# Performance work log

Hardware: AMD Instinct MI355X
Metric: run time of the kernel (lower is better)

The kernel has to match this reference:

```python
import jax, jax.numpy as jnp
import numpy as np

B, N, D = 16, 4096, 64  # (batch*heads, seq_len, head_dim)

def setup_inputs() -> dict:
    key = jax.random.key(0)
    kq, kk, kv = jax.random.split(key, 3)
    queries = jax.random.normal(kq, (B, N, D), dtype=jnp.float32)
    keys = jax.random.normal(kk, (B, N, D), dtype=jnp.float32)
    values = jax.random.normal(kv, (B, N, D), dtype=jnp.float32)
    masking = jnp.zeros((B, N), dtype=jnp.float32)
    return {"queries": queries, "keys": keys, "values": values, "masking": masking}

def reference(queries, keys, values, masking):
    # Faithful to source: masks() computes the additive mask but returns
    # `inputs` unchanged (bug in original), so `masking` is a no-op.
    d = queries.shape[-1]
    scores = jnp.einsum('bnd,bmd->bnm', queries, keys) / jnp.sqrt(jnp.float32(d))
    attn = jax.nn.softmax(scores, axis=-1)
    # Dropout(rate=0) at inference is identity.
    out = jnp.einsum('bnm,bmd->bnd', attn, values)
    return out
```

## Files before the change

### kernel.cpp

```cpp
#include <hip/hip_runtime.h>
#include <hip/hip_bf16.h>

#define B_    16
#define N_    4096
#define D_    64
#define QBLK  256
#define KVBLK 64
#define KTILES (N_ / KVBLK)

typedef __attribute__((ext_vector_type(8))) short short8v;
typedef __attribute__((ext_vector_type(4))) float f32x4;
typedef __attribute__((ext_vector_type(4))) unsigned uint4v;

__device__ __forceinline__ short f2bf(float x) {
    union { float f; unsigned u; } c; c.f = x;
    unsigned r = c.u + 0x7FFFu + ((c.u >> 16) & 1u);
    return (short)(r >> 16);
}
__device__ __forceinline__ unsigned cvtpk(float lo, float hi) {
    unsigned r;
    asm("v_cvt_pk_bf16_f32 %0, %1, %2" : "=v"(r) : "v"(lo), "v"(hi));
    return r;
}
__device__ __forceinline__ float fexp2(float x) {
    float r;
    asm("v_exp_f32 %0, %1" : "=v"(r) : "v"(x));
    return r;
}

#define GLDS16(g, l)                                                      \
    __builtin_amdgcn_global_load_lds(                                     \
        (const __attribute__((address_space(1))) void*)(g),               \
        (__attribute__((address_space(3))) void*)(l), 16, 0, 0)

__global__ __launch_bounds__(256) void conv_k(const float* __restrict__ K,
                                              short* __restrict__ Kp) {
    const int idx  = blockIdx.x * 256 + threadIdx.x;
    const int nout = idx >> 3;
    const int c8   = (idx & 7) << 3;
    const int p    = nout & 63;
    const int sig  = (p & 3) | (((p >> 4) & 1) << 2) |
                     (((p >> 2) & 3) << 3) | ((p >> 5) << 5);
    const int nsrc = (nout & ~63) | sig;
    const float* src = K + (size_t)nsrc * D_ + c8;
    const f32x4 a = *(const f32x4*)src;
    const f32x4 b = *(const f32x4*)(src + 4);
    short8v o;
    o[0] = f2bf(a[0]); o[1] = f2bf(a[1]); o[2] = f2bf(a[2]); o[3] = f2bf(a[3]);
    o[4] = f2bf(b[0]); o[5] = f2bf(b[1]); o[6] = f2bf(b[2]); o[7] = f2bf(b[3]);
    const int cs = c8 ^ ((p & 7) << 3);
    *(short8v*)(Kp + (size_t)nout * D_ + cs) = o;
}

__global__ __launch_bounds__(256) void conv_v(const float* __restrict__ V,
                                              short* __restrict__ Vp) {
    __shared__ short Tl[64][68];
    const int b  = blockIdx.x >> 6;
    const int n0 = (blockIdx.x & 63) * 64;
    const int t  = threadIdx.x;
    const int r  = t >> 2;
    const int c0 = (t & 3) * 16;
    const float* src = V + ((size_t)b * N_ + n0 + r) * D_ + c0;
    const f32x4 v0 = *(const f32x4*)(src);
    const f32x4 v1 = *(const f32x4*)(src + 4);
    const f32x4 v2 = *(const f32x4*)(src + 8);
    const f32x4 v3 = *(const f32x4*)(src + 12);
    short8v lo, hi;
    lo[0]=f2bf(v0[0]); lo[1]=f2bf(v0[1]); lo[2]=f2bf(v0[2]); lo[3]=f2bf(v0[3]);
    lo[4]=f2bf(v1[0]); lo[5]=f2bf(v1[1]); lo[6]=f2bf(v1[2]); lo[7]=f2bf(v1[3]);
    hi[0]=f2bf(v2[0]); hi[1]=f2bf(v2[1]); hi[2]=f2bf(v2[2]); hi[3]=f2bf(v2[3]);
    hi[4]=f2bf(v3[0]); hi[5]=f2bf(v3[1]); hi[6]=f2bf(v3[2]); hi[7]=f2bf(v3[3]);
    *(short8v*)&Tl[r][c0]     = lo;
    *(short8v*)&Tl[r][c0 + 8] = hi;
    __syncthreads();
    const int d  = t >> 2;
    const int nb = (t & 3) * 16;
    const int s  = (d & 7) << 3;
    short8v o0, o1;
    #pragma unroll
    for (int j = 0; j < 8; ++j) {
        o0[j] = Tl[nb + j][d];
        o1[j] = Tl[nb + 8 + j][d];
    }
    short* dst = Vp + ((size_t)b * D_ + d) * N_ + n0;
    *(short8v*)(dst + (nb ^ s))       = o0;
    *(short8v*)(dst + ((nb + 8) ^ s)) = o1;
}

__global__ __launch_bounds__(256, 1) void attn_fwd(
    const float* __restrict__ Qg, const short* __restrict__ Kp,
    const short* __restrict__ Vp, float* __restrict__ Og)
{
    __shared__ __align__(16) short Kl[4][KVBLK][D_];
    __shared__ __align__(16) short Vl[4][D_][KVBLK];

    const int tid  = threadIdx.x;
    const int w    = tid >> 6;
    const int lane = tid & 63;
    const int g    = lane >> 4;
    const int r16  = lane & 15;

    const int wg    = (blockIdx.x & 7) * 32 + (blockIdx.x >> 3);
    const int batch = wg >> 4;
    const int q0    = (wg & 15) * QBLK;

    const float SC = 0.18033688011112042f;
    short8v qf[4][2];
    #pragma unroll
    for (int q = 0; q < 4; ++q) {
        const float* qrow =
            Qg + ((size_t)batch * N_ + q0 + 64 * w + 16 * q + r16) * D_;
        #pragma unroll
        for (int c = 0; c < 2; ++c) {
            const f32x4 a0 = *(const f32x4*)(qrow + 32 * c + 8 * g);
            const f32x4 a1 = *(const f32x4*)(qrow + 32 * c + 8 * g + 4);
            short8v f;
            f[0] = f2bf(a0[0] * SC); f[1] = f2bf(a0[1] * SC);
            f[2] = f2bf(a0[2] * SC); f[3] = f2bf(a0[3] * SC);
            f[4] = f2bf(a1[0] * SC); f[5] = f2bf(a1[1] * SC);
            f[6] = f2bf(a1[2] * SC); f[7] = f2bf(a1[3] * SC);
            qf[q][c] = f;
        }
    }

    f32x4 o[4][4];
    #pragma unroll
    for (int q = 0; q < 4; ++q)
        #pragma unroll
        for (int dt = 0; dt < 4; ++dt) o[q][dt] = (f32x4){0.f, 0.f, 0.f, 0.f};
    float l[4] = {0.f, 0.f, 0.f, 0.f};
    const f32x4 Z4 = (f32x4){0.f, 0.f, 0.f, 0.f};

    const short* kbase = Kp + (size_t)batch * N_ * D_;
    const short* vbase = Vp + (size_t)batch * D_ * (size_t)N_;
    const int    swz   = (r16 & 7) << 3;
    const int    vrow  = (lane >> 3);
    const int    vcol  = (lane & 7) * 8;

#define STAGE(bb, kt_)                                                        \
    {                                                                         \
        const int kv0_ = (kt_) * KVBLK;                                       \
        _Pragma("unroll")                                                     \
        for (int j = 0; j < 2; ++j) {                                         \
            const short* gk = kbase + (size_t)kv0_ * D_ + w * 1024 + j * 512 + lane * 8; \
            GLDS16(gk, (short*)Kl[bb] + w * 1024 + j * 512);                  \
            const int dr_ = w * 16 + j * 8 + vrow;                            \
            const short* gv = vbase + (size_t)dr_ * N_ + kv0_ + vcol;         \
            GLDS16(gv, (short*)Vl[bb] + w * 1024 + j * 512);                  \
        }                                                                     \
    }

#define COMPUTE(bb)                                                           \
    {                                                                         \
        f32x4 s[4][4];   \
        __builtin_amdgcn_s_setprio(1);                                        \
        _Pragma("unroll")                                                     \
        for (int n = 0; n < 4; ++n) {                                         \
            const short8v kf0 = *(const short8v*)                             \
                &Kl[bb][r16 + 16 * n][(8 * g) ^ swz];                         \
            _Pragma("unroll")                                                 \
            for (int q = 0; q < 4; ++q)                                       \
                s[q][n] = __builtin_amdgcn_mfma_f32_16x16x32_bf16(            \
                    kf0, qf[q][0], Z4, 0, 0, 0);                              \
        }                                                                     \
        _Pragma("unroll")                                                     \
        for (int n = 0; n < 4; ++n) {                                         \
            const short8v kf1 = *(const short8v*)                             \
                &Kl[bb][r16 + 16 * n][(32 + 8 * g) ^ swz];                    \
            _Pragma("unroll")                                                 \
            for (int q = 0; q < 4; ++q)                                       \
                s[q][n] = __builtin_amdgcn_mfma_f32_16x16x32_bf16(            \
                    kf1, qf[q][1], s[q][n], 0, 0, 0);                         \
        }                                                                     \
        __builtin_amdgcn_s_setprio(0);                                        \
        _Pragma("unroll")                                                     \
        for (int q = 0; q < 4; ++q)                                           \
            _Pragma("unroll")                                                 \
            for (int n = 0; n < 4; ++n)                                       \
                _Pragma("unroll")                                             \
                for (int i = 0; i < 4; ++i)                                   \
                    s[q][n][i] = fexp2(s[q][n][i]);                           \
        _Pragma("unroll")                                                     \
        for (int q = 0; q < 4; ++q) {                                         \
            float t0 = (s[q][0][0] + s[q][0][1]) + (s[q][0][2] + s[q][0][3]); \
            float t1 = (s[q][1][0] + s[q][1][1]) + (s[q][1][2] + s[q][1][3]); \
            float t2 = (s[q][2][0] + s[q][2][1]) + (s[q][2][2] + s[q][2][3]); \
            float t3 = (s[q][3][0] + s[q][3][1]) + (s[q][3][2] + s[q][3][3]); \
            l[q] += (t0 + t1) + (t2 + t3);                                    \
        }                                                                     \
        union { uint4v u; short8v v; } f0[4], f1[4];                          \
        _Pragma("unroll")                                                     \
        for (int q = 0; q < 4; ++q) {                                         \
            f0[q].u[0] = cvtpk(s[q][0][0], s[q][0][1]);                       \
            f0[q].u[1] = cvtpk(s[q][0][2], s[q][0][3]);                       \
            f0[q].u[2] = cvtpk(s[q][1][0], s[q][1][1]);                       \
            f0[q].u[3] = cvtpk(s[q][1][2], s[q][1][3]);                       \
            f1[q].u[0] = cvtpk(s[q][2][0], s[q][2][1]);                       \
            f1[q].u[1] = cvtpk(s[q][2][2], s[q][2][3]);                       \
            f1[q].u[2] = cvtpk(s[q][3][0], s[q][3][1]);                       \
            f1[q].u[3] = cvtpk(s[q][3][2], s[q][3][3]);                       \
        }                                                                     \
        __builtin_amdgcn_s_setprio(1);                                        \
        _Pragma("unroll")                                                     \
        for (int dt = 0; dt < 4; ++dt) {                                      \
            const short8v vf = *(const short8v*)                              \
                &Vl[bb][16 * dt + r16][(8 * g) ^ swz];                        \
            _Pragma("unroll")                                                 \
            for (int q = 0; q < 4; ++q)                                       \
                o[q][dt] = __builtin_amdgcn_mfma_f32_16x16x32_bf16(           \
                    vf, f0[q].v, o[q][dt], 0, 0, 0);                          \
        }                                                                     \
        _Pragma("unroll")                                                     \
        for (int dt = 0; dt < 4; ++dt) {                                      \
            const short8v vf = *(const short8v*)                              \
                &Vl[bb][16 * dt + r16][(32 + 8 * g) ^ swz];                   \
            _Pragma("unroll")                                                 \
            for (int q = 0; q < 4; ++q)                                       \
                o[q][dt] = __builtin_amdgcn_mfma_f32_16x16x32_bf16(           \
                    vf, f1[q].v, o[q][dt], 0, 0, 0);                          \
        }                                                                     \
        __builtin_amdgcn_s_setprio(0);                                        \
    }

    STAGE(0, 0);
    STAGE(1, 1);

    const int so = w & 1;

    for (int kt = 0; kt < KTILES; kt += 2) {
        asm volatile("s_waitcnt vmcnt(0)" ::: "memory");
        __builtin_amdgcn_s_barrier();
        asm volatile("" ::: "memory");

        if (kt + 2 < KTILES) {
            STAGE((kt + 2) & 3, kt + 2);
            STAGE((kt + 3) & 3, kt + 3);
        }

        COMPUTE((kt + so) & 3);
        COMPUTE((kt + (so ^ 1)) & 3);
    }

    #pragma unroll
    for (int q = 0; q < 4; ++q) {
        l[q] += __shfl_xor(l[q], 16);
        l[q] += __shfl_xor(l[q], 32);
    }
    #pragma unroll
    for (int q = 0; q < 4; ++q) {
        const float inv = 1.0f / l[q];
        float* ob =
            Og + ((size_t)batch * N_ + q0 + 64 * w + 16 * q + r16) * D_;
        #pragma unroll
        for (int dt = 0; dt < 4; ++dt) {
            f32x4 r = o[q][dt];
            r[0] *= inv; r[1] *= inv; r[2] *= inv; r[3] *= inv;
            *(f32x4*)(ob + 16 * dt + 4 * g) = r;
        }
    }
#undef STAGE
#undef COMPUTE
}

extern "C" void kernel_launch(void* const* d_in, const int* in_sizes, int n_in,
                              void* d_out, int out_size, void* d_ws, size_t ws_size,
                              hipStream_t stream) {
    const float* Qg = (const float*)d_in[0];
    const float* Kg = (const float*)d_in[1];
    const float* Vg = (const float*)d_in[2];
    float* Og = (float*)d_out;

    const size_t nelem = (size_t)B_ * N_ * D_;
    short* Kp = (short*)d_ws;
    short* Vp = Kp + nelem;

    conv_k<<<dim3(B_ * N_ * 8 / 256), dim3(256), 0, stream>>>(Kg, Kp);
    conv_v<<<dim3(B_ * (N_ / 64)), dim3(256), 0, stream>>>(Vg, Vp);
    attn_fwd<<<dim3(B_ * (N_ / QBLK)), dim3(256), 0, stream>>>(Qg, Kp, Vp, Og);
}
```

Measured before the change: 110.6 us.

## Split KV range across two blocks per query tile and combine partials

The attention kernel now splits the key/value sequence into two halves, launching twice as many blocks with launch bounds allowing two blocks per CU. Each half writes unnormalized partial outputs and row sums, and a new combine kernel adds the halves and normalizes. The goal is more concurrent work per CU to hide latency. In exchange it adds extra global traffic for a partial output buffer plus a second kernel launch, and tighter register limits from the two-blocks-per-CU bound. The combine assumes both halves share the same softmax scaling.

```diff
diff --git a/kernel.cpp b/kernel.cpp
--- a/kernel.cpp
+++ b/kernel.cpp
@@ -87,9 +87,11 @@
     *(short8v*)(dst + ((nb + 8) ^ s)) = o1;
 }
 
-__global__ __launch_bounds__(256, 1) void attn_fwd(
+__global__ __launch_bounds__(256, 2) void attn_sp(
     const float* __restrict__ Qg, const short* __restrict__ Kp,
-    const short* __restrict__ Vp, float* __restrict__ Og)
+    const short* __restrict__ Vp, float* __restrict__ Op0,
+    float* __restrict__ Op1, float* __restrict__ l0,
+    float* __restrict__ l1, int ktn, int partial)
 {
     __shared__ __align__(16) short Kl[4][KVBLK][D_];
     __shared__ __align__(16) short Vl[4][D_][KVBLK];
@@ -100,9 +102,13 @@
     const int g    = lane >> 4;
     const int r16  = lane & 15;
 
-    const int wg    = (blockIdx.x & 7) * 32 + (blockIdx.x >> 3);
-    const int batch = wg >> 4;
-    const int q0    = (wg & 15) * QBLK;
+    const int cpx  = gridDim.x >> 3;
+    const int wg   = (blockIdx.x & 7) * cpx + (blockIdx.x >> 3);
+    const int half = wg >> 8;
+    const int rest = wg & 255;
+    const int batch = rest >> 4;
+    const int q0    = (rest & 15) * QBLK;
+    const int kt0   = half * ktn;
 
     const float SC = 0.18033688011112042f;
     short8v qf[4][2];
@@ -222,23 +228,23 @@
         __builtin_amdgcn_s_setprio(0);                                        \
     }
 
-    STAGE(0, 0);
-    STAGE(1, 1);
+    STAGE(0, kt0);
+    STAGE(1, kt0 + 1);
 
     const int so = w & 1;
 
-    for (int kt = 0; kt < KTILES; kt += 2) {
+    for (int lt = 0; lt < ktn; lt += 2) {
         asm volatile("s_waitcnt vmcnt(0)" ::: "memory");
         __builtin_amdgcn_s_barrier();
         asm volatile("" ::: "memory");
 
-        if (kt + 2 < KTILES) {
-            STAGE((kt + 2) & 3, kt + 2);
-            STAGE((kt + 3) & 3, kt + 3);
+        if (lt + 2 < ktn) {
+            STAGE((lt + 2) & 3, kt0 + lt + 2);
+            STAGE((lt + 3) & 3, kt0 + lt + 3);
         }
 
-        COMPUTE((kt + so) & 3);
-        COMPUTE((kt + (so ^ 1)) & 3);
+        COMPUTE((lt + so) & 3);
+        COMPUTE((lt + (so ^ 1)) & 3);
     }
 
     #pragma unroll
@@ -246,20 +252,54 @@
         l[q] += __shfl_xor(l[q], 16);
         l[q] += __shfl_xor(l[q], 32);
     }
-    #pragma unroll
-    for (int q = 0; q < 4; ++q) {
-        const float inv = 1.0f / l[q];
-        float* ob =
-            Og + ((size_t)batch * N_ + q0 + 64 * w + 16 * q + r16) * D_;
+    if (partial) {
+        float* Op = half ? Op1 : Op0;
+        float* lp = half ? l1 : l0;
         #pragma unroll
-        for (int dt = 0; dt < 4; ++dt) {
-            f32x4 r = o[q][dt];
-            r[0] *= inv; r[1] *= inv; r[2] *= inv; r[3] *= inv;
-            *(f32x4*)(ob + 16 * dt + 4 * g) = r;
+        for (int q = 0; q < 4; ++q) {
+            const int row = batch * N_ + q0 + 64 * w + 16 * q + r16;
+            if (g == 0) lp[row] = l[q];
+            float* ob = Op + (size_t)row * D_;
+            #pragma unroll
+            for (int dt = 0; dt < 4; ++dt)
+                *(f32x4*)(ob + 16 * dt + 4 * g) = o[q][dt];
+        }
+    } else {
+        #pragma unroll
+        for (int q = 0; q < 4; ++q) {
+            const float inv = 1.0f / l[q];
+            float* ob = Op0 +
+                ((size_t)batch * N_ + q0 + 64 * w + 16 * q + r16) * D_;
+            #pragma unroll
+            for (int dt = 0; dt < 4; ++dt) {
+                f32x4 r = o[q][dt];
+                r[0] *= inv; r[1] *= inv; r[2] *= inv; r[3] *= inv;
+                *(f32x4*)(ob + 16 * dt + 4 * g) = r;
+            }
         }
     }
 #undef STAGE
 #undef COMPUTE
+}
+
+__global__ __launch_bounds__(256) void combine_k(
+    const float* __restrict__ o1, const float* __restrict__ l0,
+    const float* __restrict__ l1, float* __restrict__ out)
+{
+    const int total = (B_ * N_ * D_) / 4;
+    for (int idx = blockIdx.x * 256 + threadIdx.x; idx < total;
+         idx += gridDim.x * 256) {
+        const int row = idx >> 4;
+        const f32x4 a = ((const f32x4*)out)[idx];
+        const f32x4 b = ((const f32x4*)o1)[idx];
+        const float inv = 1.0f / (l0[row] + l1[row]);
+        f32x4 r;
+        r[0] = (a[0] + b[0]) * inv;
+        r[1] = (a[1] + b[1]) * inv;
+        r[2] = (a[2] + b[2]) * inv;
+        r[3] = (a[3] + b[3]) * inv;
+        ((f32x4*)out)[idx] = r;
+    }
 }
 
 extern "C" void kernel_launch(void* const* d_in, const int* in_sizes, int n_in,
@@ -273,8 +313,20 @@
     const size_t nelem = (size_t)B_ * N_ * D_;
     short* Kp = (short*)d_ws;
     short* Vp = Kp + nelem;
+    float* o1 = (float*)(Vp + nelem);
+    float* l0 = o1 + nelem;
+    float* l1 = l0 + (size_t)B_ * N_;
+    const size_t need = nelem * 2 * 2 + nelem * 4 + (size_t)B_ * N_ * 4 * 2;
 
     conv_k<<<dim3(B_ * N_ * 8 / 256), dim3(256), 0, stream>>>(Kg, Kp);
     conv_v<<<dim3(B_ * (N_ / 64)), dim3(256), 0, stream>>>(Vg, Vp);
-    attn_fwd<<<dim3(B_ * (N_ / QBLK)), dim3(256), 0, stream>>>(Qg, Kp, Vp, Og);
-}
+
+    if (ws_size >= need) {
+        attn_sp<<<dim3(512), dim3(256), 0, stream>>>(
+            Qg, Kp, Vp, Og, o1, l0, l1, KTILES / 2, 1);
+        combine_k<<<dim3(1024), dim3(256), 0, stream>>>(o1, l0, l1, Og);
+    } else {
+        attn_sp<<<dim3(256), dim3(256), 0, stream>>>(
+            Qg, Kp, Vp, Og, nullptr, nullptr, nullptr, KTILES, 0);
+    }
+}
```

After: 163.2 us. 47.6% more time.
